# Performance work log

Measured on AMD Instinct MI355X. Metric: run time of the kernel, lower is better.

The kernel has to match this reference:

```python
import jax, jax.numpy as jnp
import numpy as np

B, N, D, H = 2, 512, 256, 8
HD = D // H
DFF = 4 * D
EPS = 1e-5


def layer_norm(x, g, b):
    m = jnp.mean(x, axis=-1, keepdims=True)
    v = jnp.mean(jnp.square(x - m), axis=-1, keepdims=True)
    return (x - m) * jax.lax.rsqrt(v + EPS) * g + b


def setup_inputs() -> dict:
    key = jax.random.key(0)
    ks = jax.random.split(key, 16)
    s = 0.02
    return {
        "node_features": jax.random.normal(ks[0], (B, N, D), jnp.float32),
        "edge_features": jax.random.normal(ks[1], (B, N, N, D), jnp.float32),
        "adjacency_mask": jax.random.randint(ks[2], (B, N, N), 0, 2, jnp.int32),
        "node_norm_g": jnp.ones((D,), jnp.float32),
        "node_norm_b": jnp.zeros((D,), jnp.float32),
        "edge_norm_g": jnp.ones((D,), jnp.float32),
        "edge_norm_b": jnp.zeros((D,), jnp.float32),
        "Wq": jax.random.normal(ks[3], (D, D), jnp.float32) * s,
        "bq": jnp.zeros((D,), jnp.float32),
        "Wk": jax.random.normal(ks[4], (D, D), jnp.float32) * s,
        "bk": jnp.zeros((D,), jnp.float32),
        "Wv": jax.random.normal(ks[5], (D, D), jnp.float32) * s,
        "bv": jnp.zeros((D,), jnp.float32),
        "Wo": jax.random.normal(ks[6], (D, D), jnp.float32) * s,
        "bo": jnp.zeros((D,), jnp.float32),
        "We": jax.random.normal(ks[7], (D, H), jnp.float32) * s,
        "be": jnp.zeros((H,), jnp.float32),
        "ff_norm_g": jnp.ones((D,), jnp.float32),
        "ff_norm_b": jnp.zeros((D,), jnp.float32),
        "W1": jax.random.normal(ks[8], (D, DFF), jnp.float32) * s,
        "b1": jnp.zeros((DFF,), jnp.float32),
        "W2": jax.random.normal(ks[9], (DFF, D), jnp.float32) * s,
        "b2": jnp.zeros((D,), jnp.float32),
    }


def reference(node_features, edge_features, adjacency_mask,
              node_norm_g, node_norm_b, edge_norm_g, edge_norm_b,
              Wq, bq, Wk, bk, Wv, bv, Wo, bo, We, be,
              ff_norm_g, ff_norm_b, W1, b1, W2, b2):
    x = node_features
    nn_ = layer_norm(x, node_norm_g, node_norm_b)
    # project and split heads: (B, H, N, HD)
    q = (nn_ @ Wq + bq).reshape(B, N, H, HD).transpose(0, 2, 1, 3)
    k = (nn_ @ Wk + bk).reshape(B, N, H, HD).transpose(0, 2, 1, 3)
    v = (nn_ @ Wv + bv).reshape(B, N, H, HD).transpose(0, 2, 1, 3)
    scores = jnp.einsum('bhnd,bhmd->bhnm', q, k) / jnp.sqrt(jnp.float32(HD))
    # edge bias: LayerNorm over D then Linear(D->H), move H first
    eb = layer_norm(edge_features, edge_norm_g, edge_norm_b) @ We + be  # (B,N,N,H)
    scores = scores + eb.transpose(0, 3, 1, 2)
    scores = jnp.where(adjacency_mask[:, None, :, :] == 0, -jnp.inf, scores)
    attn = jax.nn.softmax(scores, axis=-1)
    out = jnp.einsum('bhnm,bhmd->bhnd', attn, v)
    out = out.transpose(0, 2, 1, 3).reshape(B, N, D) @ Wo + bo
    x = x + out
    # feedforward (dropout is identity at inference)
    h = layer_norm(x, ff_norm_g, ff_norm_b)
    h = jax.nn.gelu(h @ W1 + b1, approximate=False) @ W2 + b2
    return x + h
```

## Files before the change

### kernel.cpp

```cpp
#include <hip/hip_runtime.h>
#include <hip/hip_bf16.h>

typedef unsigned int uint;

constexpr float EPS_ = 1e-5f;

#define DEV __device__ __forceinline__

DEV float gelu_(float x){ return 0.5f*x*(1.f + erff(x*0.70710678118654752f)); }

__global__ __launch_bounds__(256) void k_qkv(
    const float* __restrict__ x,
    const float* __restrict__ g, const float* __restrict__ bta,
    const float* __restrict__ Wq, const float* __restrict__ bq,
    const float* __restrict__ Wk, const float* __restrict__ bk,
    const float* __restrict__ Wv, const float* __restrict__ bv,
    const float* __restrict__ eg, const float* __restrict__ ebb,
    const float* __restrict__ We, const float* __restrict__ be,
    float* __restrict__ GW, float* __restrict__ Av, float* __restrict__ Cv,
    float* __restrict__ q, float* __restrict__ k, float* __restrict__ v)
{
    const int t = threadIdx.x;
    __shared__ float redA2[4][8];
    __shared__ float redC2[4][8];
    if (blockIdx.x == 0) {
        float gd = eg[t], bd = ebb[t];
        float a_loc[8], c_loc[8];
        #pragma unroll
        for (int h = 0; h < 8; ++h) {
            float w = We[t*8 + h];
            float gw = gd * w;
            GW[t*8 + h] = gw;
            a_loc[h] = gw;
            c_loc[h] = bd * w;
        }
        #pragma unroll
        for (int h = 0; h < 8; ++h) {
            #pragma unroll
            for (int o = 32; o >= 1; o >>= 1) {
                a_loc[h] += __shfl_xor(a_loc[h], o);
                c_loc[h] += __shfl_xor(c_loc[h], o);
            }
        }
        if ((t & 63) == 0) {
            const int w = t >> 6;
            #pragma unroll
            for (int h = 0; h < 8; ++h) { redA2[w][h] = a_loc[h]; redC2[w][h] = c_loc[h]; }
        }
        __syncthreads();
        if (t < 8) {
            Av[t] = redA2[0][t] + redA2[1][t] + redA2[2][t] + redA2[3][t];
            Cv[t] = redC2[0][t] + redC2[1][t] + redC2[2][t] + redC2[3][t] + be[t];
        }
    }

    const int wid = t >> 6, l = t & 63;
    const int r0 = blockIdx.x << 1;
    __shared__ float sxT[256*2];
    if (wid < 2) {
        const int row = r0 + wid;
        const float4 xv4 = ((const float4*)x)[row*64 + l];
        float s  = xv4.x + xv4.y + xv4.z + xv4.w;
        float q2 = xv4.x*xv4.x + xv4.y*xv4.y + xv4.z*xv4.z + xv4.w*xv4.w;
        #pragma unroll
        for (int o = 32; o >= 1; o >>= 1) { s += __shfl_xor(s, o); q2 += __shfl_xor(q2, o); }
        const float m = s * (1.f/256.f);
        const float rinv = rsqrtf(q2*(1.f/256.f) - m*m + EPS_);
        const float4 g4 = ((const float4*)g)[l];
        const float4 b4 = ((const float4*)bta)[l];
        sxT[(4*l+0)*2 + wid] = (xv4.x - m)*rinv*g4.x + b4.x;
        sxT[(4*l+1)*2 + wid] = (xv4.y - m)*rinv*g4.y + b4.y;
        sxT[(4*l+2)*2 + wid] = (xv4.z - m)*rinv*g4.z + b4.z;
        sxT[(4*l+3)*2 + wid] = (xv4.w - m)*rinv*g4.w + b4.w;
    }
    __syncthreads();
    float aq0 = bq[t], ak0 = bk[t], av0 = bv[t];
    float aq1 = aq0, ak1 = ak0, av1 = av0;
    for (int d = 0; d < 256; d += 2) {
        const float4 s4 = *((const float4*)&sxT[d*2]);
        const float wqa = Wq[d*256 + t], wqb = Wq[(d+1)*256 + t];
        const float wka = Wk[d*256 + t], wkb = Wk[(d+1)*256 + t];
        const float wva = Wv[d*256 + t], wvb = Wv[(d+1)*256 + t];
        aq0 = fmaf(s4.x, wqa, aq0); aq0 = fmaf(s4.z, wqb, aq0);
        aq1 = fmaf(s4.y, wqa, aq1); aq1 = fmaf(s4.w, wqb, aq1);
        ak0 = fmaf(s4.x, wka, ak0); ak0 = fmaf(s4.z, wkb, ak0);
        ak1 = fmaf(s4.y, wka, ak1); ak1 = fmaf(s4.w, wkb, ak1);
        av0 = fmaf(s4.x, wva, av0); av0 = fmaf(s4.z, wvb, av0);
        av1 = fmaf(s4.y, wva, av1); av1 = fmaf(s4.w, wvb, av1);
    }
    q[(r0+0)*256 + t] = aq0; q[(r0+1)*256 + t] = aq1;
    k[(r0+0)*256 + t] = ak0; k[(r0+1)*256 + t] = ak1;
    v[(r0+0)*256 + t] = av0; v[(r0+1)*256 + t] = av1;
}

__global__ __launch_bounds__(256, 5) void k_eattn(
    const float4* __restrict__ ep,
    const int*   __restrict__ msk,
    const float* __restrict__ GWg, const float* __restrict__ Avec, const float* __restrict__ Cvec,
    const float* __restrict__ qg, const float4* __restrict__ kg4, const float* __restrict__ vg,
    float* __restrict__ ao)
{
    __shared__ float smem[5120];
    __shared__ float sqv[256];
    __shared__ float sden[8];
    const int t = threadIdx.x;
    const int bi = blockIdx.x;
    const int b = bi >> 9;
    sqv[t] = qg[(size_t)bi*256 + t] * 0.17677669529663687f;
    __syncthreads();

    const int r = t >> 2, u = t & 3;

    float S[2][8], qk[2][8], mval[2], rinv[2], mb[2];

    #pragma unroll
    for (int half = 0; half < 2; ++half) {
        const long long rowBase = ((long long)bi << 9) + (half << 8);
        const int krow0 = (b << 9) + (half << 8);
        float sum = 0.f, ssq = 0.f;
        #pragma unroll
        for (int h = 0; h < 8; ++h) { S[half][h] = 0.f; qk[half][h] = 0.f; }

        for (int c = 0; c < 16; ++c) {
            *((float4*)&smem[(r      )*20 + (u << 2)]) = ep[(rowBase + r      )*64 + (c << 2) + u];
            *((float4*)&smem[(r +  64)*20 + (u << 2)]) = ep[(rowBase + r +  64)*64 + (c << 2) + u];
            *((float4*)&smem[(r + 128)*20 + (u << 2)]) = ep[(rowBase + r + 128)*64 + (c << 2) + u];
            *((float4*)&smem[(r + 192)*20 + (u << 2)]) = ep[(rowBase + r + 192)*64 + (c << 2) + u];
            __syncthreads();
            const float* srow = &smem[t*20];
            const int d0 = c << 4;
            #pragma unroll
            for (int j4 = 0; j4 < 4; ++j4) {
                const float4 e4 = *((const float4*)&srow[j4 << 2]);
                #pragma unroll
                for (int uu = 0; uu < 4; ++uu) {
                    const float e = (uu==0) ? e4.x : (uu==1) ? e4.y : (uu==2) ? e4.z : e4.w;
                    const float* gw = &GWg[(size_t)(d0 + (j4 << 2) + uu) << 3];
                    sum += e;
                    ssq = fmaf(e, e, ssq);
                    S[half][0] = fmaf(e, gw[0], S[half][0]); S[half][1] = fmaf(e, gw[1], S[half][1]);
                    S[half][2] = fmaf(e, gw[2], S[half][2]); S[half][3] = fmaf(e, gw[3], S[half][3]);
                    S[half][4] = fmaf(e, gw[4], S[half][4]); S[half][5] = fmaf(e, gw[5], S[half][5]);
                    S[half][6] = fmaf(e, gw[6], S[half][6]); S[half][7] = fmaf(e, gw[7], S[half][7]);
                }
            }
            __syncthreads();
        }

        for (int c = 0; c < 16; ++c) {
            *((float4*)&smem[(r      )*20 + (u << 2)]) = kg4[(size_t)(krow0 + r      )*64 + (c << 2) + u];
            *((float4*)&smem[(r +  64)*20 + (u << 2)]) = kg4[(size_t)(krow0 + r +  64)*64 + (c << 2) + u];
            *((float4*)&smem[(r + 128)*20 + (u << 2)]) = kg4[(size_t)(krow0 + r + 128)*64 + (c << 2) + u];
            *((float4*)&smem[(r + 192)*20 + (u << 2)]) = kg4[(size_t)(krow0 + r + 192)*64 + (c << 2) + u];
            __syncthreads();
            const float* srow = &smem[t*20];
            const float4* q4p = (const float4*)&sqv[c << 4];
            float acc = qk[half][c >> 1];
            #pragma unroll
            for (int j4 = 0; j4 < 4; ++j4) {
                const float4 k4 = *((const float4*)&srow[j4 << 2]);
                const float4 q4 = q4p[j4];
                acc = fmaf(k4.x, q4.x, acc); acc = fmaf(k4.y, q4.y, acc);
                acc = fmaf(k4.z, q4.z, acc); acc = fmaf(k4.w, q4.w, acc);
            }
            qk[half][c >> 1] = acc;
            __syncthreads();
        }

        mval[half] = sum * (1.f/256.f);
        rinv[half] = rsqrtf(ssq*(1.f/256.f) - mval[half]*mval[half] + EPS_);
        mb[half]   = (msk[rowBase + t] == 0) ? -1e30f : 0.f;
    }

    float* sb = smem;
    #pragma unroll
    for (int half = 0; half < 2; ++half) {
        const int jrow = (half << 8) + t;
        #pragma unroll
        for (int h = 0; h < 8; ++h)
            sb[h*512 + jrow] = qk[half][h]
                             + rinv[half] * (S[half][h] - mval[half] * Avec[h])
                             + Cvec[h] + mb[half];
    }
    __syncthreads();

    {
        const int h = t >> 5, l = t & 31;
        float* base = &sb[h*512 + (l << 4)];
        float4 s4[4];
        float pmax = -3.0e38f;
        #pragma unroll
        for (int i = 0; i < 4; ++i) {
            s4[i] = *((const float4*)&base[i << 2]);
            pmax = fmaxf(pmax, fmaxf(fmaxf(s4[i].x, s4[i].y), fmaxf(s4[i].z, s4[i].w)));
        }
        #pragma unroll
        for (int o = 16; o >= 1; o >>= 1) pmax = fmaxf(pmax, __shfl_xor(pmax, o));
        float psum = 0.f;
        #pragma unroll
        for (int i = 0; i < 4; ++i) {
            const float p0 = __expf(s4[i].x - pmax), p1 = __expf(s4[i].y - pmax);
            const float p2 = __expf(s4[i].z - pmax), p3 = __expf(s4[i].w - pmax);
            psum += (p0 + p1) + (p2 + p3);
            *((float4*)&base[i << 2]) = make_float4(p0, p1, p2, p3);
        }
        #pragma unroll
        for (int o = 16; o >= 1; o >>= 1) psum += __shfl_xor(psum, o);
        if (l == 0) sden[h] = psum;
    }
    __syncthreads();

    {
        const int h = t >> 5;
        const float* vb = vg + ((size_t)b << 9)*256 + t;
        const float4* spr4 = (const float4*)&sb[h*512];
        float a0 = 0.f, a1 = 0.f, a2 = 0.f, a3 = 0.f;
        for (int j4 = 0; j4 < 128; ++j4) {
            const float4 p4 = spr4[j4];
            const float* vj = vb + ((size_t)j4 << 2)*256;
            a0 = fmaf(p4.x, vj[0],   a0);
            a1 = fmaf(p4.y, vj[256], a1);
            a2 = fmaf(p4.z, vj[512], a2);
            a3 = fmaf(p4.w, vj[768], a3);
        }
        ao[(size_t)bi*256 + t] = (a0+a1+a2+a3) / sden[h];
    }
}

__global__ __launch_bounds__(256) void k_projff(
    const float* __restrict__ at, const float* __restrict__ Wo,
    const float* __restrict__ bo, const float* __restrict__ x,
    const float* __restrict__ g, const float* __restrict__ bb,
    const float* __restrict__ W1, const float* __restrict__ b1,
    const float* __restrict__ W2, const float* __restrict__ b2,
    float* __restrict__ out)
{
    const int t = threadIdx.x;
    const int wid = t >> 6, l = t & 63;
    const int r0 = blockIdx.x << 1;
    __shared__ float saT[256*2];
    __shared__ float shT[256*2];
    __shared__ float sfT[2*1024];
    __shared__ float sx1[2][256];

    if (wid < 2) {
        const float4 a4 = ((const float4*)at)[(r0 + wid)*64 + l];
        saT[(4*l+0)*2 + wid] = a4.x;
        saT[(4*l+1)*2 + wid] = a4.y;
        saT[(4*l+2)*2 + wid] = a4.z;
        saT[(4*l+3)*2 + wid] = a4.w;
    }
    __syncthreads();
    {
        float A0 = bo[t], A1 = A0;
        for (int d = 0; d < 256; d += 2) {
            const float4 s4 = *((const float4*)&saT[d*2]);
            const float wa = Wo[d*256 + t], wb = Wo[(d+1)*256 + t];
            A0 = fmaf(s4.x, wa, A0); A0 = fmaf(s4.z, wb, A0);
            A1 = fmaf(s4.y, wa, A1); A1 = fmaf(s4.w, wb, A1);
        }
        sx1[0][t] = A0 + x[(r0+0)*256 + t];
        sx1[1][t] = A1 + x[(r0+1)*256 + t];
    }
    __syncthreads();
    if (wid < 2) {
        const float4 xv4 = *((const float4*)&sx1[wid][4*l]);
        float s  = xv4.x + xv4.y + xv4.z + xv4.w;
        float q2 = xv4.x*xv4.x + xv4.y*xv4.y + xv4.z*xv4.z + xv4.w*xv4.w;
        #pragma unroll
        for (int o = 32; o >= 1; o >>= 1) { s += __shfl_xor(s, o); q2 += __shfl_xor(q2, o); }
        const float m = s * (1.f/256.f);
        const float rinv = rsqrtf(q2*(1.f/256.f) - m*m + EPS_);
        const float4 g4 = ((const float4*)g)[l];
        const float4 b4 = ((const float4*)bb)[l];
        shT[(4*l+0)*2 + wid] = (xv4.x - m)*rinv*g4.x + b4.x;
        shT[(4*l+1)*2 + wid] = (xv4.y - m)*rinv*g4.y + b4.y;
        shT[(4*l+2)*2 + wid] = (xv4.z - m)*rinv*g4.z + b4.z;
        shT[(4*l+3)*2 + wid] = (xv4.w - m)*rinv*g4.w + b4.w;
    }
    __syncthreads();
    {
        const float4 bc = ((const float4*)b1)[t];
        float A00 = bc.x, A01 = bc.x;
        float A10 = bc.y, A11 = bc.y;
        float A20 = bc.z, A21 = bc.z;
        float A30 = bc.w, A31 = bc.w;
        const float4* W14 = (const float4*)W1;
        for (int d = 0; d < 256; ++d) {
            const float2 s2 = *((const float2*)&shT[d*2]);
            const float4 w4 = W14[d*256 + t];
            A00 = fmaf(s2.x, w4.x, A00); A01 = fmaf(s2.y, w4.x, A01);
            A10 = fmaf(s2.x, w4.y, A10); A11 = fmaf(s2.y, w4.y, A11);
            A20 = fmaf(s2.x, w4.z, A20); A21 = fmaf(s2.y, w4.z, A21);
            A30 = fmaf(s2.x, w4.w, A30); A31 = fmaf(s2.y, w4.w, A31);
        }
        *((float4*)&sfT[0*1024 + 4*t]) = make_float4(gelu_(A00), gelu_(A10), gelu_(A20), gelu_(A30));
        *((float4*)&sfT[1*1024 + 4*t]) = make_float4(gelu_(A01), gelu_(A11), gelu_(A21), gelu_(A31));
    }
    __syncthreads();
    {
        float AO0 = b2[t], AO1 = AO0;
        for (int kk = 0; kk < 1024; ++kk) {
            const float w = W2[kk*256 + t];
            AO0 = fmaf(sfT[kk],        w, AO0);
            AO1 = fmaf(sfT[1024 + kk], w, AO1);
        }
        out[(r0+0)*256 + t] = AO0 + sx1[0][t];
        out[(r0+1)*256 + t] = AO1 + sx1[1][t];
    }
}

extern "C" void kernel_launch(void* const* d_in, const int* in_sizes, int n_in,
                              void* d_out, int out_size, void* d_ws, size_t ws_size,
                              hipStream_t stream) {
    const float* x   = (const float*)d_in[0];
    const float* ef  = (const float*)d_in[1];
    const int*   am  = (const int*)d_in[2];
    const float* ng  = (const float*)d_in[3];
    const float* nb  = (const float*)d_in[4];
    const float* eg  = (const float*)d_in[5];
    const float* ebb = (const float*)d_in[6];
    const float* Wq  = (const float*)d_in[7];
    const float* bq  = (const float*)d_in[8];
    const float* Wk  = (const float*)d_in[9];
    const float* bk  = (const float*)d_in[10];
    const float* Wv  = (const float*)d_in[11];
    const float* bv  = (const float*)d_in[12];
    const float* Wo  = (const float*)d_in[13];
    const float* bo  = (const float*)d_in[14];
    const float* We  = (const float*)d_in[15];
    const float* be  = (const float*)d_in[16];
    const float* fg  = (const float*)d_in[17];
    const float* fb  = (const float*)d_in[18];
    const float* W1  = (const float*)d_in[19];
    const float* b1  = (const float*)d_in[20];
    const float* W2  = (const float*)d_in[21];
    const float* b2  = (const float*)d_in[22];

    float* ws  = (float*)d_ws;
    float* GW  = ws;
    float* Av  = ws + 2048;
    float* Cv  = ws + 2064;
    float* q   = ws + 4096;
    float* k   = q  + 262144;
    float* v   = k  + 262144;
    float* ao  = v  + 262144;

    hipLaunchKernelGGL(k_qkv, dim3(512), dim3(256), 0, stream,
                       x, ng, nb, Wq, bq, Wk, bk, Wv, bv,
                       eg, ebb, We, be, GW, Av, Cv, q, k, v);
    hipLaunchKernelGGL(k_eattn, dim3(1024), dim3(256), 0, stream,
                       (const float4*)ef, am, GW, Av, Cv, q, (const float4*)k, v, ao);
    hipLaunchKernelGGL(k_projff, dim3(512), dim3(256), 0, stream,
                       ao, Wo, bo, x, fg, fb, W1, b1, W2, b2, (float*)d_out);
}
```

Measured before the change: 271.8 us.

## Widen edge-attention staging chunks and process four rows per FFN block

```diff
diff --git a/kernel.cpp b/kernel.cpp
--- a/kernel.cpp
+++ b/kernel.cpp
@@ -93,14 +93,14 @@
     v[(r0+0)*256 + t] = av0; v[(r0+1)*256 + t] = av1;
 }
 
-__global__ __launch_bounds__(256, 5) void k_eattn(
+__global__ __launch_bounds__(256, 4) void k_eattn(
     const float4* __restrict__ ep,
     const int*   __restrict__ msk,
     const float* __restrict__ GWg, const float* __restrict__ Avec, const float* __restrict__ Cvec,
     const float* __restrict__ qg, const float4* __restrict__ kg4, const float* __restrict__ vg,
     float* __restrict__ ao)
 {
-    __shared__ float smem[5120];
+    __shared__ float smem[256*36];
     __shared__ float sqv[256];
     __shared__ float sden[8];
     const int t = threadIdx.x;
@@ -121,16 +121,18 @@
         #pragma unroll
         for (int h = 0; h < 8; ++h) { S[half][h] = 0.f; qk[half][h] = 0.f; }
 
-        for (int c = 0; c < 16; ++c) {
-            *((float4*)&smem[(r      )*20 + (u << 2)]) = ep[(rowBase + r      )*64 + (c << 2) + u];
-            *((float4*)&smem[(r +  64)*20 + (u << 2)]) = ep[(rowBase + r +  64)*64 + (c << 2) + u];
-            *((float4*)&smem[(r + 128)*20 + (u << 2)]) = ep[(rowBase + r + 128)*64 + (c << 2) + u];
-            *((float4*)&smem[(r + 192)*20 + (u << 2)]) = ep[(rowBase + r + 192)*64 + (c << 2) + u];
+        for (int c = 0; c < 8; ++c) {
+            #pragma unroll
+            for (int rr = 0; rr < 4; ++rr) {
+                const int row = r + (rr << 6);
+                *((float4*)&smem[row*36 + (u << 2)])       = ep[(rowBase + row)*64 + (c << 3) + u];
+                *((float4*)&smem[row*36 + ((u+4) << 2)])   = ep[(rowBase + row)*64 + (c << 3) + u + 4];
+            }
             __syncthreads();
-            const float* srow = &smem[t*20];
-            const int d0 = c << 4;
-            #pragma unroll
-            for (int j4 = 0; j4 < 4; ++j4) {
+            const float* srow = &smem[t*36];
+            const int d0 = c << 5;
+            #pragma unroll
+            for (int j4 = 0; j4 < 8; ++j4) {
                 const float4 e4 = *((const float4*)&srow[j4 << 2]);
                 #pragma unroll
                 for (int uu = 0; uu < 4; ++uu) {
@@ -147,23 +149,25 @@
             __syncthreads();
         }
 
-        for (int c = 0; c < 16; ++c) {
-            *((float4*)&smem[(r      )*20 + (u << 2)]) = kg4[(size_t)(krow0 + r      )*64 + (c << 2) + u];
-            *((float4*)&smem[(r +  64)*20 + (u << 2)]) = kg4[(size_t)(krow0 + r +  64)*64 + (c << 2) + u];
-            *((float4*)&smem[(r + 128)*20 + (u << 2)]) = kg4[(size_t)(krow0 + r + 128)*64 + (c << 2) + u];
-            *((float4*)&smem[(r + 192)*20 + (u << 2)]) = kg4[(size_t)(krow0 + r + 192)*64 + (c << 2) + u];
+        for (int c = 0; c < 8; ++c) {
+            #pragma unroll
+            for (int rr = 0; rr < 4; ++rr) {
+                const int row = r + (rr << 6);
+                *((float4*)&smem[row*36 + (u << 2)])       = kg4[(size_t)(krow0 + row)*64 + (c << 3) + u];
+                *((float4*)&smem[row*36 + ((u+4) << 2)])   = kg4[(size_t)(krow0 + row)*64 + (c << 3) + u + 4];
+            }
             __syncthreads();
-            const float* srow = &smem[t*20];
-            const float4* q4p = (const float4*)&sqv[c << 4];
-            float acc = qk[half][c >> 1];
-            #pragma unroll
-            for (int j4 = 0; j4 < 4; ++j4) {
+            const float* srow = &smem[t*36];
+            const float4* q4p = (const float4*)&sqv[c << 5];
+            float acc = qk[half][c];
+            #pragma unroll
+            for (int j4 = 0; j4 < 8; ++j4) {
                 const float4 k4 = *((const float4*)&srow[j4 << 2]);
                 const float4 q4 = q4p[j4];
                 acc = fmaf(k4.x, q4.x, acc); acc = fmaf(k4.y, q4.y, acc);
                 acc = fmaf(k4.z, q4.z, acc); acc = fmaf(k4.w, q4.w, acc);
             }
-            qk[half][c >> 1] = acc;
+            qk[half][c] = acc;
             __syncthreads();
         }
 
@@ -237,33 +241,36 @@
 {
     const int t = threadIdx.x;
     const int wid = t >> 6, l = t & 63;
-    const int r0 = blockIdx.x << 1;
-    __shared__ float saT[256*2];
-    __shared__ float shT[256*2];
-    __shared__ float sfT[2*1024];
-    __shared__ float sx1[2][256];
-
-    if (wid < 2) {
+    const int r0 = blockIdx.x << 2;
+    __shared__ float saT[256*4];
+    __shared__ float shT[256*4];
+    __shared__ float sfT[1024*4];
+    __shared__ float sx1[4][256];
+
+    {
         const float4 a4 = ((const float4*)at)[(r0 + wid)*64 + l];
-        saT[(4*l+0)*2 + wid] = a4.x;
-        saT[(4*l+1)*2 + wid] = a4.y;
-        saT[(4*l+2)*2 + wid] = a4.z;
-        saT[(4*l+3)*2 + wid] = a4.w;
-    }
-    __syncthreads();
-    {
-        float A0 = bo[t], A1 = A0;
-        for (int d = 0; d < 256; d += 2) {
-            const float4 s4 = *((const float4*)&saT[d*2]);
-            const float wa = Wo[d*256 + t], wb = Wo[(d+1)*256 + t];
-            A0 = fmaf(s4.x, wa, A0); A0 = fmaf(s4.z, wb, A0);
-            A1 = fmaf(s4.y, wa, A1); A1 = fmaf(s4.w, wb, A1);
+        saT[(4*l+0)*4 + wid] = a4.x;
+        saT[(4*l+1)*4 + wid] = a4.y;
+        saT[(4*l+2)*4 + wid] = a4.z;
+        saT[(4*l+3)*4 + wid] = a4.w;
+    }
+    __syncthreads();
+    {
+        const float bov = bo[t];
+        float A0 = bov, A1 = bov, A2 = bov, A3 = bov;
+        for (int d = 0; d < 256; ++d) {
+            const float4 s4 = *((const float4*)&saT[d*4]);
+            const float wo = Wo[d*256 + t];
+            A0 = fmaf(s4.x, wo, A0); A1 = fmaf(s4.y, wo, A1);
+            A2 = fmaf(s4.z, wo, A2); A3 = fmaf(s4.w, wo, A3);
         }
         sx1[0][t] = A0 + x[(r0+0)*256 + t];
         sx1[1][t] = A1 + x[(r0+1)*256 + t];
-    }
-    __syncthreads();
-    if (wid < 2) {
+        sx1[2][t] = A2 + x[(r0+2)*256 + t];
+        sx1[3][t] = A3 + x[(r0+3)*256 + t];
+    }
+    __syncthreads();
+    {
         const float4 xv4 = *((const float4*)&sx1[wid][4*l]);
         float s  = xv4.x + xv4.y + xv4.z + xv4.w;
         float q2 = xv4.x*xv4.x + xv4.y*xv4.y + xv4.z*xv4.z + xv4.w*xv4.w;
@@ -273,40 +280,50 @@
         const float rinv = rsqrtf(q2*(1.f/256.f) - m*m + EPS_);
         const float4 g4 = ((const float4*)g)[l];
         const float4 b4 = ((const float4*)bb)[l];
-        shT[(4*l+0)*2 + wid] = (xv4.x - m)*rinv*g4.x + b4.x;
-        shT[(4*l+1)*2 + wid] = (xv4.y - m)*rinv*g4.y + b4.y;
-        shT[(4*l+2)*2 + wid] = (xv4.z - m)*rinv*g4.z + b4.z;
-        shT[(4*l+3)*2 + wid] = (xv4.w - m)*rinv*g4.w + b4.w;
+        shT[(4*l+0)*4 + wid] = (xv4.x - m)*rinv*g4.x + b4.x;
+        shT[(4*l+1)*4 + wid] = (xv4.y - m)*rinv*g4.y + b4.y;
+        shT[(4*l+2)*4 + wid] = (xv4.z - m)*rinv*g4.z + b4.z;
+        shT[(4*l+3)*4 + wid] = (xv4.w - m)*rinv*g4.w + b4.w;
     }
     __syncthreads();
     {
         const float4 bc = ((const float4*)b1)[t];
-        float A00 = bc.x, A01 = bc.x;
-        float A10 = bc.y, A11 = bc.y;
-        float A20 = bc.z, A21 = bc.z;
-        float A30 = bc.w, A31 = bc.w;
+        float A00=bc.x, A01=bc.x, A02=bc.x, A03=bc.x;
+        float A10=bc.y, A11=bc.y, A12=bc.y, A13=bc.y;
+        float A20=bc.z, A21=bc.z, A22=bc.z, A23=bc.z;
+        float A30=bc.w, A31=bc.w, A32=bc.w, A33=bc.w;
         const float4* W14 = (const float4*)W1;
         for (int d = 0; d < 256; ++d) {
-            const float2 s2 = *((const float2*)&shT[d*2]);
+            const float4 s4 = *((const float4*)&shT[d*4]);
             const float4 w4 = W14[d*256 + t];
-            A00 = fmaf(s2.x, w4.x, A00); A01 = fmaf(s2.y, w4.x, A01);
-            A10 = fmaf(s2.x, w4.y, A10); A11 = fmaf(s2.y, w4.y, A11);
-            A20 = fmaf(s2.x, w4.z, A20); A21 = fmaf(s2.y, w4.z, A21);
-            A30 = fmaf(s2.x, w4.w, A30); A31 = fmaf(s2.y, w4.w, A31);
-        }
-        *((float4*)&sfT[0*1024 + 4*t]) = make_float4(gelu_(A00), gelu_(A10), gelu_(A20), gelu_(A30));
-        *((float4*)&sfT[1*1024 + 4*t]) = make_float4(gelu_(A01), gelu_(A11), gelu_(A21), gelu_(A31));
-    }
-    __syncthreads();
-    {
-        float AO0 = b2[t], AO1 = AO0;
+            A00 = fmaf(s4.x, w4.x, A00); A01 = fmaf(s4.y, w4.x, A01);
+            A02 = fmaf(s4.z, w4.x, A02); A03 = fmaf(s4.w, w4.x, A03);
+            A10 = fmaf(s4.x, w4.y, A10); A11 = fmaf(s4.y, w4.y, A11);
+            A12 = fmaf(s4.z, w4.y, A12); A13 = fmaf(s4.w, w4.y, A13);
+            A20 = fmaf(s4.x, w4.z, A20); A21 = fmaf(s4.y, w4.z, A21);
+            A22 = fmaf(s4.z, w4.z, A22); A23 = fmaf(s4.w, w4.z, A23);
+            A30 = fmaf(s4.x, w4.w, A30); A31 = fmaf(s4.y, w4.w, A31);
+            A32 = fmaf(s4.z, w4.w, A32); A33 = fmaf(s4.w, w4.w, A33);
+        }
+        *((float4*)&sfT[(4*t+0)*4]) = make_float4(gelu_(A00), gelu_(A01), gelu_(A02), gelu_(A03));
+        *((float4*)&sfT[(4*t+1)*4]) = make_float4(gelu_(A10), gelu_(A11), gelu_(A12), gelu_(A13));
+        *((float4*)&sfT[(4*t+2)*4]) = make_float4(gelu_(A20), gelu_(A21), gelu_(A22), gelu_(A23));
+        *((float4*)&sfT[(4*t+3)*4]) = make_float4(gelu_(A30), gelu_(A31), gelu_(A32), gelu_(A33));
+    }
+    __syncthreads();
+    {
+        const float b2v = b2[t];
+        float AO0 = b2v, AO1 = b2v, AO2 = b2v, AO3 = b2v;
         for (int kk = 0; kk < 1024; ++kk) {
+            const float4 s4 = *((const float4*)&sfT[kk*4]);
             const float w = W2[kk*256 + t];
-            AO0 = fmaf(sfT[kk],        w, AO0);
-            AO1 = fmaf(sfT[1024 + kk], w, AO1);
+            AO0 = fmaf(s4.x, w, AO0); AO1 = fmaf(s4.y, w, AO1);
+            AO2 = fmaf(s4.z, w, AO2); AO3 = fmaf(s4.w, w, AO3);
         }
         out[(r0+0)*256 + t] = AO0 + sx1[0][t];
         out[(r0+1)*256 + t] = AO1 + sx1[1][t];
+        out[(r0+2)*256 + t] = AO2 + sx1[2][t];
+        out[(r0+3)*256 + t] = AO3 + sx1[3][t];
     }
 }
 
@@ -351,6 +368,6 @@
                        eg, ebb, We, be, GW, Av, Cv, q, k, v);
     hipLaunchKernelGGL(k_eattn, dim3(1024), dim3(256), 0, stream,
                        (const float4*)ef, am, GW, Av, Cv, q, (const float4*)k, v, ao);
-    hipLaunchKernelGGL(k_projff, dim3(512), dim3(256), 0, stream,
+    hipLaunchKernelGGL(k_projff, dim3(256), dim3(256), 0, stream,
                        ao, Wo, bo, x, fg, fb, W1, b1, W2, b2, (float*)d_out);
 }
```

Measured after the change: 288.8 us. 6.3% more time.

## Split edge-bias computation into its own kernel ahead of attention

Applied to the files above, without the earlier changes.

```diff
diff --git a/kernel.cpp b/kernel.cpp
--- a/kernel.cpp
+++ b/kernel.cpp
@@ -93,11 +93,64 @@
     v[(r0+0)*256 + t] = av0; v[(r0+1)*256 + t] = av1;
 }
 
-__global__ __launch_bounds__(256, 5) void k_eattn(
+__global__ __launch_bounds__(256, 8) void k_edge(
     const float4* __restrict__ ep,
     const int*   __restrict__ msk,
     const float* __restrict__ GWg, const float* __restrict__ Avec, const float* __restrict__ Cvec,
-    const float* __restrict__ qg, const float4* __restrict__ kg4, const float* __restrict__ vg,
+    float* __restrict__ eb)
+{
+    __shared__ float smem[256*20];
+    const int t = threadIdx.x;
+    const long long rowBase = (long long)blockIdx.x << 8;
+    const int r = t >> 2, u = t & 3;
+
+    float sum = 0.f, ssq = 0.f;
+    float S[8] = {0.f,0.f,0.f,0.f,0.f,0.f,0.f,0.f};
+
+    for (int c = 0; c < 16; ++c) {
+        *((float4*)&smem[(r      )*20 + (u << 2)]) = ep[(rowBase + r      )*64 + (c << 2) + u];
+        *((float4*)&smem[(r +  64)*20 + (u << 2)]) = ep[(rowBase + r +  64)*64 + (c << 2) + u];
+        *((float4*)&smem[(r + 128)*20 + (u << 2)]) = ep[(rowBase + r + 128)*64 + (c << 2) + u];
+        *((float4*)&smem[(r + 192)*20 + (u << 2)]) = ep[(rowBase + r + 192)*64 + (c << 2) + u];
+        __syncthreads();
+        const float* srow = &smem[t*20];
+        const int d0 = c << 4;
+        #pragma unroll
+        for (int j4 = 0; j4 < 4; ++j4) {
+            const float4 e4 = *((const float4*)&srow[j4 << 2]);
+            #pragma unroll
+            for (int uu = 0; uu < 4; ++uu) {
+                const float e = (uu==0) ? e4.x : (uu==1) ? e4.y : (uu==2) ? e4.z : e4.w;
+                const float* gw = &GWg[(size_t)(d0 + (j4 << 2) + uu) << 3];
+                sum += e;
+                ssq = fmaf(e, e, ssq);
+                S[0] = fmaf(e, gw[0], S[0]); S[1] = fmaf(e, gw[1], S[1]);
+                S[2] = fmaf(e, gw[2], S[2]); S[3] = fmaf(e, gw[3], S[3]);
+                S[4] = fmaf(e, gw[4], S[4]); S[5] = fmaf(e, gw[5], S[5]);
+                S[6] = fmaf(e, gw[6], S[6]); S[7] = fmaf(e, gw[7], S[7]);
+            }
+        }
+        __syncthreads();
+    }
+
+    const long long grow = rowBase + t;
+    const float m = sum * (1.f/256.f);
+    const float rinv = rsqrtf(ssq*(1.f/256.f) - m*m + EPS_);
+    const int mk = msk[grow];
+    const int b = (int)(grow >> 18);
+    const int rem = (int)(grow & ((1 << 18) - 1));
+    float* ebp = eb + ((long long)b << 21) + rem;
+    #pragma unroll
+    for (int h = 0; h < 8; ++h) {
+        float val = rinv * (S[h] - m * Avec[h]) + Cvec[h];
+        if (mk == 0) val = -1e30f;
+        ebp[(long long)h << 18] = val;
+    }
+}
+
+__global__ __launch_bounds__(256, 6) void k_attn(
+    const float* __restrict__ ebt,
+    const float4* __restrict__ kg4, const float* __restrict__ qg, const float* __restrict__ vg,
     float* __restrict__ ao)
 {
     __shared__ float smem[5120];
@@ -105,48 +158,17 @@
     __shared__ float sden[8];
     const int t = threadIdx.x;
     const int bi = blockIdx.x;
-    const int b = bi >> 9;
+    const int b = bi >> 9, i = bi & 511;
     sqv[t] = qg[(size_t)bi*256 + t] * 0.17677669529663687f;
     __syncthreads();
 
     const int r = t >> 2, u = t & 3;
-
-    float S[2][8], qk[2][8], mval[2], rinv[2], mb[2];
-
+    float qk[2][8];
     #pragma unroll
     for (int half = 0; half < 2; ++half) {
-        const long long rowBase = ((long long)bi << 9) + (half << 8);
+        #pragma unroll
+        for (int h = 0; h < 8; ++h) qk[half][h] = 0.f;
         const int krow0 = (b << 9) + (half << 8);
-        float sum = 0.f, ssq = 0.f;
-        #pragma unroll
-        for (int h = 0; h < 8; ++h) { S[half][h] = 0.f; qk[half][h] = 0.f; }
-
-        for (int c = 0; c < 16; ++c) {
-            *((float4*)&smem[(r      )*20 + (u << 2)]) = ep[(rowBase + r      )*64 + (c << 2) + u];
-            *((float4*)&smem[(r +  64)*20 + (u << 2)]) = ep[(rowBase + r +  64)*64 + (c << 2) + u];
-            *((float4*)&smem[(r + 128)*20 + (u << 2)]) = ep[(rowBase + r + 128)*64 + (c << 2) + u];
-            *((float4*)&smem[(r + 192)*20 + (u << 2)]) = ep[(rowBase + r + 192)*64 + (c << 2) + u];
-            __syncthreads();
-            const float* srow = &smem[t*20];
-            const int d0 = c << 4;
-            #pragma unroll
-            for (int j4 = 0; j4 < 4; ++j4) {
-                const float4 e4 = *((const float4*)&srow[j4 << 2]);
-                #pragma unroll
-                for (int uu = 0; uu < 4; ++uu) {
-                    const float e = (uu==0) ? e4.x : (uu==1) ? e4.y : (uu==2) ? e4.z : e4.w;
-                    const float* gw = &GWg[(size_t)(d0 + (j4 << 2) + uu) << 3];
-                    sum += e;
-                    ssq = fmaf(e, e, ssq);
-                    S[half][0] = fmaf(e, gw[0], S[half][0]); S[half][1] = fmaf(e, gw[1], S[half][1]);
-                    S[half][2] = fmaf(e, gw[2], S[half][2]); S[half][3] = fmaf(e, gw[3], S[half][3]);
-                    S[half][4] = fmaf(e, gw[4], S[half][4]); S[half][5] = fmaf(e, gw[5], S[half][5]);
-                    S[half][6] = fmaf(e, gw[6], S[half][6]); S[half][7] = fmaf(e, gw[7], S[half][7]);
-                }
-            }
-            __syncthreads();
-        }
-
         for (int c = 0; c < 16; ++c) {
             *((float4*)&smem[(r      )*20 + (u << 2)]) = kg4[(size_t)(krow0 + r      )*64 + (c << 2) + u];
             *((float4*)&smem[(r +  64)*20 + (u << 2)]) = kg4[(size_t)(krow0 + r +  64)*64 + (c << 2) + u];
@@ -166,21 +188,16 @@
             qk[half][c >> 1] = acc;
             __syncthreads();
         }
-
-        mval[half] = sum * (1.f/256.f);
-        rinv[half] = rsqrtf(ssq*(1.f/256.f) - mval[half]*mval[half] + EPS_);
-        mb[half]   = (msk[rowBase + t] == 0) ? -1e30f : 0.f;
     }
 
     float* sb = smem;
+    const float* ebbase = ebt + ((long long)b << 21) + (size_t)i*512;
     #pragma unroll
     for (int half = 0; half < 2; ++half) {
         const int jrow = (half << 8) + t;
         #pragma unroll
         for (int h = 0; h < 8; ++h)
-            sb[h*512 + jrow] = qk[half][h]
-                             + rinv[half] * (S[half][h] - mval[half] * Avec[h])
-                             + Cvec[h] + mb[half];
+            sb[h*512 + jrow] = qk[half][h] + ebbase[((long long)h << 18) + jrow];
     }
     __syncthreads();
 
@@ -190,19 +207,19 @@
         float4 s4[4];
         float pmax = -3.0e38f;
         #pragma unroll
-        for (int i = 0; i < 4; ++i) {
-            s4[i] = *((const float4*)&base[i << 2]);
-            pmax = fmaxf(pmax, fmaxf(fmaxf(s4[i].x, s4[i].y), fmaxf(s4[i].z, s4[i].w)));
+        for (int ii = 0; ii < 4; ++ii) {
+            s4[ii] = *((const float4*)&base[ii << 2]);
+            pmax = fmaxf(pmax, fmaxf(fmaxf(s4[ii].x, s4[ii].y), fmaxf(s4[ii].z, s4[ii].w)));
         }
         #pragma unroll
         for (int o = 16; o >= 1; o >>= 1) pmax = fmaxf(pmax, __shfl_xor(pmax, o));
         float psum = 0.f;
         #pragma unroll
-        for (int i = 0; i < 4; ++i) {
-            const float p0 = __expf(s4[i].x - pmax), p1 = __expf(s4[i].y - pmax);
-            const float p2 = __expf(s4[i].z - pmax), p3 = __expf(s4[i].w - pmax);
+        for (int ii = 0; ii < 4; ++ii) {
+            const float p0 = __expf(s4[ii].x - pmax), p1 = __expf(s4[ii].y - pmax);
+            const float p2 = __expf(s4[ii].z - pmax), p3 = __expf(s4[ii].w - pmax);
             psum += (p0 + p1) + (p2 + p3);
-            *((float4*)&base[i << 2]) = make_float4(p0, p1, p2, p3);
+            *((float4*)&base[ii << 2]) = make_float4(p0, p1, p2, p3);
         }
         #pragma unroll
         for (int o = 16; o >= 1; o >>= 1) psum += __shfl_xor(psum, o);
@@ -345,12 +362,15 @@
     float* k   = q  + 262144;
     float* v   = k  + 262144;
     float* ao  = v  + 262144;
+    float* ebt = ao + 262144;
 
     hipLaunchKernelGGL(k_qkv, dim3(512), dim3(256), 0, stream,
                        x, ng, nb, Wq, bq, Wk, bk, Wv, bv,
                        eg, ebb, We, be, GW, Av, Cv, q, k, v);
-    hipLaunchKernelGGL(k_eattn, dim3(1024), dim3(256), 0, stream,
-                       (const float4*)ef, am, GW, Av, Cv, q, (const float4*)k, v, ao);
+    hipLaunchKernelGGL(k_edge, dim3(2048), dim3(256), 0, stream,
+                       (const float4*)ef, am, GW, Av, Cv, ebt);
+    hipLaunchKernelGGL(k_attn, dim3(1024), dim3(256), 0, stream,
+                       ebt, (const float4*)k, q, v, ao);
     hipLaunchKernelGGL(k_projff, dim3(512), dim3(256), 0, stream,
                        ao, Wo, bo, x, fg, fb, W1, b1, W2, b2, (float*)d_out);
 }
```

Result: slower. 307.3 us (+13.1%).

## Double-buffer edge and key tiles in LDS with register prefetch

Applied to the files above, without the earlier changes.

```diff
diff --git a/kernel.cpp b/kernel.cpp
--- a/kernel.cpp
+++ b/kernel.cpp
@@ -93,14 +93,14 @@
     v[(r0+0)*256 + t] = av0; v[(r0+1)*256 + t] = av1;
 }
 
-__global__ __launch_bounds__(256, 5) void k_eattn(
+__global__ __launch_bounds__(256, 4) void k_eattn(
     const float4* __restrict__ ep,
     const int*   __restrict__ msk,
     const float* __restrict__ GWg, const float* __restrict__ Avec, const float* __restrict__ Cvec,
     const float* __restrict__ qg, const float4* __restrict__ kg4, const float* __restrict__ vg,
     float* __restrict__ ao)
 {
-    __shared__ float smem[5120];
+    __shared__ float smem[8704];
     __shared__ float sqv[256];
     __shared__ float sden[8];
     const int t = threadIdx.x;
@@ -110,6 +110,7 @@
     __syncthreads();
 
     const int r = t >> 2, u = t & 3;
+    const int wr0 = r*17 + (u << 2);
 
     float S[2][8], qk[2][8], mval[2], rinv[2], mb[2];
 
@@ -121,49 +122,74 @@
         #pragma unroll
         for (int h = 0; h < 8; ++h) { S[half][h] = 0.f; qk[half][h] = 0.f; }
 
-        for (int c = 0; c < 16; ++c) {
-            *((float4*)&smem[(r      )*20 + (u << 2)]) = ep[(rowBase + r      )*64 + (c << 2) + u];
-            *((float4*)&smem[(r +  64)*20 + (u << 2)]) = ep[(rowBase + r +  64)*64 + (c << 2) + u];
-            *((float4*)&smem[(r + 128)*20 + (u << 2)]) = ep[(rowBase + r + 128)*64 + (c << 2) + u];
-            *((float4*)&smem[(r + 192)*20 + (u << 2)]) = ep[(rowBase + r + 192)*64 + (c << 2) + u];
-            __syncthreads();
-            const float* srow = &smem[t*20];
-            const int d0 = c << 4;
-            #pragma unroll
-            for (int j4 = 0; j4 < 4; ++j4) {
-                const float4 e4 = *((const float4*)&srow[j4 << 2]);
-                #pragma unroll
-                for (int uu = 0; uu < 4; ++uu) {
-                    const float e = (uu==0) ? e4.x : (uu==1) ? e4.y : (uu==2) ? e4.z : e4.w;
-                    const float* gw = &GWg[(size_t)(d0 + (j4 << 2) + uu) << 3];
-                    sum += e;
-                    ssq = fmaf(e, e, ssq);
-                    S[half][0] = fmaf(e, gw[0], S[half][0]); S[half][1] = fmaf(e, gw[1], S[half][1]);
-                    S[half][2] = fmaf(e, gw[2], S[half][2]); S[half][3] = fmaf(e, gw[3], S[half][3]);
-                    S[half][4] = fmaf(e, gw[4], S[half][4]); S[half][5] = fmaf(e, gw[5], S[half][5]);
-                    S[half][6] = fmaf(e, gw[6], S[half][6]); S[half][7] = fmaf(e, gw[7], S[half][7]);
+        float4 R0, R1, R2, R3;
+        R0 = ep[(rowBase + r      )*64 + u];
+        R1 = ep[(rowBase + r +  64)*64 + u];
+        R2 = ep[(rowBase + r + 128)*64 + u];
+        R3 = ep[(rowBase + r + 192)*64 + u];
+        {
+            float* buf = smem;
+            *((float4*)&buf[wr0          ]) = R0;
+            *((float4*)&buf[wr0 + 64*17  ]) = R1;
+            *((float4*)&buf[wr0 + 128*17 ]) = R2;
+            *((float4*)&buf[wr0 + 192*17 ]) = R3;
+        }
+        __syncthreads();
+
+        for (int cc = 0; cc < 32; ++cc) {
+            if (cc + 1 < 32) {
+                const int nc = cc + 1;
+                if (nc < 16) {
+                    R0 = ep[(rowBase + r      )*64 + (nc << 2) + u];
+                    R1 = ep[(rowBase + r +  64)*64 + (nc << 2) + u];
+                    R2 = ep[(rowBase + r + 128)*64 + (nc << 2) + u];
+                    R3 = ep[(rowBase + r + 192)*64 + (nc << 2) + u];
+                } else {
+                    const int kc = nc - 16;
+                    R0 = kg4[(size_t)(krow0 + r      )*64 + (kc << 2) + u];
+                    R1 = kg4[(size_t)(krow0 + r +  64)*64 + (kc << 2) + u];
+                    R2 = kg4[(size_t)(krow0 + r + 128)*64 + (kc << 2) + u];
+                    R3 = kg4[(size_t)(krow0 + r + 192)*64 + (kc << 2) + u];
                 }
             }
-            __syncthreads();
-        }
-
-        for (int c = 0; c < 16; ++c) {
-            *((float4*)&smem[(r      )*20 + (u << 2)]) = kg4[(size_t)(krow0 + r      )*64 + (c << 2) + u];
-            *((float4*)&smem[(r +  64)*20 + (u << 2)]) = kg4[(size_t)(krow0 + r +  64)*64 + (c << 2) + u];
-            *((float4*)&smem[(r + 128)*20 + (u << 2)]) = kg4[(size_t)(krow0 + r + 128)*64 + (c << 2) + u];
-            *((float4*)&smem[(r + 192)*20 + (u << 2)]) = kg4[(size_t)(krow0 + r + 192)*64 + (c << 2) + u];
-            __syncthreads();
-            const float* srow = &smem[t*20];
-            const float4* q4p = (const float4*)&sqv[c << 4];
-            float acc = qk[half][c >> 1];
-            #pragma unroll
-            for (int j4 = 0; j4 < 4; ++j4) {
-                const float4 k4 = *((const float4*)&srow[j4 << 2]);
-                const float4 q4 = q4p[j4];
-                acc = fmaf(k4.x, q4.x, acc); acc = fmaf(k4.y, q4.y, acc);
-                acc = fmaf(k4.z, q4.z, acc); acc = fmaf(k4.w, q4.w, acc);
+            const float* srow = &smem[(cc & 1) ? 4352 : 0] + t*17;
+            if (cc < 16) {
+                const int d0 = cc << 4;
+                #pragma unroll
+                for (int j4 = 0; j4 < 4; ++j4) {
+                    const float4 e4 = *((const float4*)&srow[j4 << 2]);
+                    #pragma unroll
+                    for (int uu = 0; uu < 4; ++uu) {
+                        const float e = (uu==0) ? e4.x : (uu==1) ? e4.y : (uu==2) ? e4.z : e4.w;
+                        const float* gw = &GWg[(size_t)(d0 + (j4 << 2) + uu) << 3];
+                        sum += e;
+                        ssq = fmaf(e, e, ssq);
+                        S[half][0] = fmaf(e, gw[0], S[half][0]); S[half][1] = fmaf(e, gw[1], S[half][1]);
+                        S[half][2] = fmaf(e, gw[2], S[half][2]); S[half][3] = fmaf(e, gw[3], S[half][3]);
+                        S[half][4] = fmaf(e, gw[4], S[half][4]); S[half][5] = fmaf(e, gw[5], S[half][5]);
+                        S[half][6] = fmaf(e, gw[6], S[half][6]); S[half][7] = fmaf(e, gw[7], S[half][7]);
+                    }
+                }
+            } else {
+                const int kc = cc - 16;
+                const float4* q4p = (const float4*)&sqv[kc << 4];
+                float acc = qk[half][kc >> 1];
+                #pragma unroll
+                for (int j4 = 0; j4 < 4; ++j4) {
+                    const float4 k4 = *((const float4*)&srow[j4 << 2]);
+                    const float4 q4 = q4p[j4];
+                    acc = fmaf(k4.x, q4.x, acc); acc = fmaf(k4.y, q4.y, acc);
+                    acc = fmaf(k4.z, q4.z, acc); acc = fmaf(k4.w, q4.w, acc);
+                }
+                qk[half][kc >> 1] = acc;
             }
-            qk[half][c >> 1] = acc;
+            if (cc + 1 < 32) {
+                float* buf = &smem[((cc + 1) & 1) ? 4352 : 0];
+                *((float4*)&buf[wr0          ]) = R0;
+                *((float4*)&buf[wr0 + 64*17  ]) = R1;
+                *((float4*)&buf[wr0 + 128*17 ]) = R2;
+                *((float4*)&buf[wr0 + 192*17 ]) = R3;
+            }
             __syncthreads();
         }
 
```

Measured after the change: 379.0 us. 39.4% more time.
